# Performance work log

Measured on AMD Instinct MI355X. Metric: run time of the kernel, lower is better.

The kernel has to match this reference:

```python
import jax, jax.numpy as jnp
import numpy as np

B, F, V = 65536, 512, 28  # batch, feature_count, vocab_size (embedding hardcoded 28x28)


def setup_inputs() -> dict:
    key = jax.random.key(0)
    ks = jax.random.split(key, 12)
    s = lambda fan_in, fan_out: (2.0 / (fan_in + fan_out)) ** 0.5  # Glorot normal std
    return {
        "inputs": jax.random.normal(ks[0], (B, F), jnp.float32),
        "prev_prediction": jax.random.randint(ks[1], (B, V), 0, V, jnp.int32),
        "prev_state": jax.random.normal(ks[2], (B, V), jnp.float32),
        # GRUCell params (keras reset_after=True: two bias rows)
        "gru_kernel": jax.random.normal(ks[3], (F, 3 * V), jnp.float32) * s(F, 3 * V),
        "gru_rkernel": jax.random.normal(ks[4], (V, 3 * V), jnp.float32) * s(V, 3 * V),
        "gru_bias": jnp.zeros((2, 3 * V), jnp.float32),
        # cascaded output projections
        "Wo": jax.random.normal(ks[5], (V, 1), jnp.float32) * s(V, 1),
        "Uo": jax.random.normal(ks[6], (V, V), jnp.float32) * s(V, V),
        "Co": jax.random.normal(ks[7], (F, V), jnp.float32) * s(F, V),
        "Bo": jax.random.normal(ks[8], (1, V), jnp.float32) * s(1, V),
        "emb": jax.random.uniform(ks[9], (V, V), jnp.float32, -0.05, 0.05),
    }


def _gru_cell(x, h, kernel, rkernel, bias):
    # keras GRUCell, reset_after=True
    xm = x @ kernel + bias[0]          # [B, 3V]
    hm = h @ rkernel + bias[1]         # [B, 3V]
    xz, xr, xh = jnp.split(xm, 3, axis=-1)
    hz, hr, hh = jnp.split(hm, 3, axis=-1)
    z = jax.nn.sigmoid(xz + hz)
    r = jax.nn.sigmoid(xr + hr)
    hcand = jnp.tanh(xh + r * hh)
    return z * h + (1.0 - z) * hcand


def reference(inputs, prev_prediction, prev_state, gru_kernel, gru_rkernel, gru_bias, Wo, Uo, Co, Bo, emb):
    gru_out = _gru_cell(inputs, prev_state, gru_kernel, gru_rkernel, gru_bias)  # [B, V]
    emb_out = emb[prev_prediction]                      # [B, V, V] (gather)
    WoY = jnp.einsum("bve,e->bv", emb_out, Wo[:, 0])    # [B, V]
    UoH = prev_state @ Uo                               # [B, V]
    CoC = inputs @ Co                                   # [B, V]
    pred = jax.nn.softmax(WoY + UoH + CoC + Bo, axis=-1)
    return pred, gru_out
```

## Files before the change

kernel.cpp:

```cpp
#include <hip/hip_runtime.h>
#include <hip/hip_bf16.h>
#include <math.h>

#define BATCH   65536
#define FDIM    512
#define VDIM    28
#define TILE_R  64
#define NKS     32
#define W1N     (NKS * 4 * 64 * 8)
#define W2N     (2 * 4 * 64 * 8)


using short8 = __attribute__((ext_vector_type(8))) short;
using f32x16 = __attribute__((ext_vector_type(16))) float;

__device__ __forceinline__ float sigmoidf_(float x) { return 1.0f / (1.0f + __expf(-x)); }
__device__ __forceinline__ float tanhf_(float x) { return 1.0f - 2.0f / (1.0f + __expf(2.0f * x)); }

__device__ __forceinline__ unsigned short f2bf_rne(float f) {
    unsigned u = __float_as_uint(f);
    u += 0x7FFFu + ((u >> 16) & 1u);
    return (unsigned short)(u >> 16);
}

__device__ __forceinline__ void split2(float f0, float f1, unsigned& hp, unsigned& lp) {
    unsigned u0 = __float_as_uint(f0), u1 = __float_as_uint(f1);
    hp = (u0 >> 16) | (u1 & 0xFFFF0000u);
    float d0 = f0 - __uint_as_float(u0 & 0xFFFF0000u);
    float d1 = f1 - __uint_as_float(u1 & 0xFFFF0000u);
    unsigned v0 = __float_as_uint(d0), v1 = __float_as_uint(d1);
    lp = (v0 >> 16) | (v1 & 0xFFFF0000u);
}

__global__ void prep_kernel(const float* __restrict__ gk, const float* __restrict__ co,
                            const float* __restrict__ rk, const float* __restrict__ uo,
                            const float* __restrict__ emb, const float* __restrict__ wo,
                            unsigned short* __restrict__ w1h, unsigned short* __restrict__ w1l,
                            unsigned short* __restrict__ w2h, unsigned short* __restrict__ w2l,
                            float* __restrict__ tt) {
    int tid = blockIdx.x * 256 + threadIdx.x;
    int nth = gridDim.x * 256;
    for (int idx = tid; idx < W1N; idx += nth) {
        int j = idx & 7, lane = (idx >> 3) & 63, nf = (idx >> 9) & 3, ks = idx >> 11;
        int k = ks * 16 + ((lane >> 5) << 3) + j;
        int v = lane & 31;
        float val = 0.0f;
        if (v < VDIM) val = (nf < 3) ? gk[k * 84 + nf * 28 + v] : co[k * VDIM + v];
        unsigned short hi = f2bf_rne(val);
        float fh = __uint_as_float(((unsigned)hi) << 16);
        w1h[idx] = hi;
        w1l[idx] = f2bf_rne(val - fh);
    }
    for (int idx = tid; idx < W2N; idx += nth) {
        int j = idx & 7, lane = (idx >> 3) & 63, nf = (idx >> 9) & 3, ks = idx >> 11;
        int k = ks * 16 + ((lane >> 5) << 3) + j;
        int v = lane & 31;
        float val = 0.0f;
        if (v < VDIM && k < VDIM) val = (nf < 3) ? rk[k * 84 + nf * 28 + v] : uo[k * VDIM + v];
        unsigned short hi = f2bf_rne(val);
        float fh = __uint_as_float(((unsigned)hi) << 16);
        w2h[idx] = hi;
        w2l[idx] = f2bf_rne(val - fh);
    }
    if (tid < VDIM) {
        float s = 0.0f;
        for (int e = 0; e < VDIM; e++) s = fmaf(emb[tid * VDIM + e], wo[e], s);
        tt[tid] = s;
    }
}

#define MFMA(A, B, C) __builtin_amdgcn_mfma_f32_32x32x16_bf16(A, B, C, 0, 0, 0)
#define SPLIT8(A0, A1, AH, AL)                                        \
    {                                                                 \
        uint4 hu_, lu_;                                               \
        split2(A0.x, A0.y, hu_.x, lu_.x);                             \
        split2(A0.z, A0.w, hu_.y, lu_.y);                             \
        split2(A1.x, A1.y, hu_.z, lu_.z);                             \
        split2(A1.z, A1.w, hu_.w, lu_.w);                             \
        AH = __builtin_bit_cast(short8, hu_);                         \
        AL = __builtin_bit_cast(short8, lu_);                         \
    }
#define MFMA4(ACC, AH, AL, BH, BL)                                    \
    ACC = MFMA(AH, BH, ACC); ACC = MFMA(AL, BH, ACC);                 \
    ACC = MFMA(AH, BL, ACC); ACC = MFMA(AL, BL, ACC);

__global__ __launch_bounds__(128, 2) void gru_main_kernel(
    const float* __restrict__ x,
    const int*   __restrict__ pp,
    const float* __restrict__ ps,
    const float* __restrict__ bias,
    const float* __restrict__ bo,
    const unsigned short* __restrict__ w1h, const unsigned short* __restrict__ w1l,
    const unsigned short* __restrict__ w2h, const unsigned short* __restrict__ w2l,
    const float* __restrict__ tt,
    float* __restrict__ out)
{
    __shared__ float hbuf[TILE_R * VDIM];
    __shared__ int   ppbuf[TILE_R * VDIM];
    __shared__ float tts[32];

    const int t = threadIdx.x;
    const int wid = t >> 6, l = t & 63;
    const int cl = l & 31, gh = l >> 5;
    const long row0 = (long)blockIdx.x * TILE_R;
    const int m0 = 32 * wid;

    for (int i = t; i < TILE_R * VDIM; i += 128) {
        hbuf[i]  = ps[row0 * VDIM + i];
        ppbuf[i] = pp[row0 * VDIM + i];
    }
    if (t < 32) tts[t] = (t < VDIM) ? tt[t] : 0.0f;

    const int vc = (cl < VDIM) ? cl : (VDIM - 1);
    const float b0z = bias[vc],      b0r = bias[28 + vc],  b0h = bias[56 + vc];
    const float b1z = bias[84 + vc], b1r = bias[112 + vc], b1h = bias[140 + vc];
    const float bov = bo[vc];

    f32x16 accz = {}, accr = {}, acch = {}, accc = {}, hacch = {};

    {
        const float* hrow = ps + (row0 + m0 + cl) * (long)VDIM;
        const short8* bh8 = (const short8*)w2h + l;
        const short8* bl8 = (const short8*)w2l + l;
        short8 ah, al, bh, bl;
        {
            float4 a0 = *(const float4*)(hrow + gh * 8);
            float4 a1 = *(const float4*)(hrow + gh * 8 + 4);
            SPLIT8(a0, a1, ah, al);
            bh = bh8[0];   bl = bl8[0];   MFMA4(accz,  ah, al, bh, bl);
            bh = bh8[64];  bl = bl8[64];  MFMA4(accr,  ah, al, bh, bl);
            bh = bh8[128]; bl = bl8[128]; MFMA4(hacch, ah, al, bh, bl);
            bh = bh8[192]; bl = bl8[192]; MFMA4(accc,  ah, al, bh, bl);
        }
        {
            float4 a0 = *(const float4*)(hrow + 16 + gh * 8);
            float4 a1 = make_float4(0.f, 0.f, 0.f, 0.f);
            if (!gh) a1 = *(const float4*)(hrow + 20);
            SPLIT8(a0, a1, ah, al);
            bh = bh8[256]; bl = bl8[256]; MFMA4(accz,  ah, al, bh, bl);
            bh = bh8[320]; bl = bl8[320]; MFMA4(accr,  ah, al, bh, bl);
            bh = bh8[384]; bl = bl8[384]; MFMA4(hacch, ah, al, bh, bl);
            bh = bh8[448]; bl = bl8[448]; MFMA4(accc,  ah, al, bh, bl);
        }
    }

    {
        const float* xrow = x + (row0 + m0 + cl) * (long)FDIM + gh * 8;
        const short8* bh8 = (const short8*)w1h + l;
        const short8* bl8 = (const short8*)w1l + l;
        #pragma unroll 4
        for (int ks = 0; ks < NKS; ++ks) {
            float4 a0 = *(const float4*)(xrow + ks * 16);
            float4 a1 = *(const float4*)(xrow + ks * 16 + 4);
            short8 ah, al, bh, bl;
            SPLIT8(a0, a1, ah, al);
            const int kb = ks * 256;
            bh = bh8[kb];       bl = bl8[kb];       MFMA4(accz, ah, al, bh, bl);
            bh = bh8[kb + 64];  bl = bl8[kb + 64];  MFMA4(accr, ah, al, bh, bl);
            bh = bh8[kb + 128]; bl = bl8[kb + 128]; MFMA4(acch, ah, al, bh, bl);
            bh = bh8[kb + 192]; bl = bl8[kb + 192]; MFMA4(accc, ah, al, bh, bl);
        }
    }

    __syncthreads();

    #pragma unroll
    for (int r = 0; r < 16; ++r) {
        const int rowf = (r & 3) + ((r >> 2) << 3) + (gh << 2);
        const int grow = m0 + rowf;
        const long orow = row0 + grow;
        const float hp  = hbuf[grow * VDIM + vc];
        const int   ppv = ppbuf[grow * VDIM + vc];

        const float z  = sigmoidf_(accz[r] + b0z + b1z);
        const float rg = sigmoidf_(accr[r] + b0r + b1r);
        const float hc = tanhf_(acch[r] + b0h + rg * (hacch[r] + b1h));
        const float go = z * hp + (1.0f - z) * hc;
        const float logit = tts[ppv & 31] + accc[r] + bov;

        float mx = (cl < VDIM) ? logit : -1e30f;
        mx = fmaxf(mx, __shfl_xor(mx, 16));
        mx = fmaxf(mx, __shfl_xor(mx, 8));
        mx = fmaxf(mx, __shfl_xor(mx, 4));
        mx = fmaxf(mx, __shfl_xor(mx, 2));
        mx = fmaxf(mx, __shfl_xor(mx, 1));
        float p = (cl < VDIM) ? __expf(logit - mx) : 0.0f;
        float s = p;
        s += __shfl_xor(s, 16);
        s += __shfl_xor(s, 8);
        s += __shfl_xor(s, 4);
        s += __shfl_xor(s, 2);
        s += __shfl_xor(s, 1);

        if (cl < VDIM) {
            out[orow * VDIM + cl] = p / s;
            out[(long)BATCH * VDIM + orow * VDIM + cl] = go;
        }
    }
}

extern "C" void kernel_launch(void* const* d_in, const int* in_sizes, int n_in,
                              void* d_out, int out_size, void* d_ws, size_t ws_size,
                              hipStream_t stream) {
    const float* x    = (const float*)d_in[0];
    const int*   pp   = (const int*)  d_in[1];
    const float* ps   = (const float*)d_in[2];
    const float* gk   = (const float*)d_in[3];
    const float* rk   = (const float*)d_in[4];
    const float* bias = (const float*)d_in[5];
    const float* wo   = (const float*)d_in[6];
    const float* uo   = (const float*)d_in[7];
    const float* co   = (const float*)d_in[8];
    const float* bo   = (const float*)d_in[9];
    const float* emb  = (const float*)d_in[10];

    unsigned short* w1h = (unsigned short*)d_ws;
    unsigned short* w1l = w1h + W1N;
    unsigned short* w2h = w1l + W1N;
    unsigned short* w2l = w2h + W2N;
    float*          tt  = (float*)(w2l + W2N);

    prep_kernel<<<64, 256, 0, stream>>>(gk, co, rk, uo, emb, wo, w1h, w1l, w2h, w2l, tt);
    gru_main_kernel<<<BATCH / TILE_R, 128, 0, stream>>>(
        x, pp, ps, bias, bo, w1h, w1l, w2h, w2l, tt, (float*)d_out);
}
```

Measured before the change: 257.3 us.

## Split K across warps and double-buffer weight tiles via global_load_lds

Doubles the block to 256 threads, with two warps per 32-row group each taking half of the 512-wide K range. Weight fragments are streamed into double-buffered LDS with async global-to-LDS loads, and x loads are prefetched one step ahead. Partial accumulators are then reduced through LDS before a single warp does the epilogue. The aim is more latency hiding and parallelism on a load-bound GEMM, at the cost of a barrier every K step plus five reduction barriers, and the epilogue now reads prev_state and prev_prediction straight from global memory.

```diff
diff --git a/kernel.cpp b/kernel.cpp
--- a/kernel.cpp
+++ b/kernel.cpp
@@ -6,10 +6,8 @@
 #define FDIM    512
 #define VDIM    28
 #define TILE_R  64
-#define NKS     32
-#define W1N     (NKS * 4 * 64 * 8)
+#define W1N     (32 * 4 * 64 * 8)
 #define W2N     (2 * 4 * 64 * 8)
-
 
 using short8 = __attribute__((ext_vector_type(8))) short;
 using f32x16 = __attribute__((ext_vector_type(16))) float;
@@ -84,7 +82,11 @@
     ACC = MFMA(AH, BH, ACC); ACC = MFMA(AL, BH, ACC);                 \
     ACC = MFMA(AH, BL, ACC); ACC = MFMA(AL, BL, ACC);
 
-__global__ __launch_bounds__(128, 2) void gru_main_kernel(
+#define GLD_LDS16(G, L) __builtin_amdgcn_global_load_lds(                         \
+    (const __attribute__((address_space(1))) void*)(G),                           \
+    (__attribute__((address_space(3))) void*)(L), 16, 0, 0)
+
+__global__ __launch_bounds__(256, 3) void gru_main_kernel(
     const float* __restrict__ x,
     const int*   __restrict__ pp,
     const float* __restrict__ ps,
@@ -95,21 +97,21 @@
     const float* __restrict__ tt,
     float* __restrict__ out)
 {
-    __shared__ float hbuf[TILE_R * VDIM];
-    __shared__ int   ppbuf[TILE_R * VDIM];
-    __shared__ float tts[32];
+    __shared__ short8 bb[2][2][2][256];
 
     const int t = threadIdx.x;
     const int wid = t >> 6, l = t & 63;
+    const int wid_m = wid & 1, wid_k = wid >> 1;
     const int cl = l & 31, gh = l >> 5;
     const long row0 = (long)blockIdx.x * TILE_R;
-    const int m0 = 32 * wid;
-
-    for (int i = t; i < TILE_R * VDIM; i += 128) {
-        hbuf[i]  = ps[row0 * VDIM + i];
-        ppbuf[i] = pp[row0 * VDIM + i];
-    }
-    if (t < 32) tts[t] = (t < VDIM) ? tt[t] : 0.0f;
+    const int m0x = 32 * wid_m;
+
+    #pragma unroll
+    for (int rr = 0; rr < 4; ++rr) {
+        const int s = rr >> 1, p = rr & 1;
+        const unsigned short* srcb = p ? w1l : w1h;
+        GLD_LDS16(srcb + (s * 16) * 2048 + t * 8, &bb[s][0][p][t]);
+    }
 
     const int vc = (cl < VDIM) ? cl : (VDIM - 1);
     const float b0z = bias[vc],      b0r = bias[28 + vc],  b0h = bias[56 + vc];
@@ -118,83 +120,114 @@
 
     f32x16 accz = {}, accr = {}, acch = {}, accc = {}, hacch = {};
 
+    const float* xrow = x + (row0 + m0x + cl) * (long)FDIM + gh * 8;
+    const int ks0 = wid_k * 16;
+    float4 a0n = *(const float4*)(xrow + ks0 * 16);
+    float4 a1n = *(const float4*)(xrow + ks0 * 16 + 4);
+
     {
-        const float* hrow = ps + (row0 + m0 + cl) * (long)VDIM;
+        const float* hrow = ps + (row0 + m0x + cl) * (long)VDIM;
         const short8* bh8 = (const short8*)w2h + l;
         const short8* bl8 = (const short8*)w2l + l;
+        float4 a0, a1;
+        if (wid_k == 0) {
+            a0 = *(const float4*)(hrow + gh * 8);
+            a1 = *(const float4*)(hrow + gh * 8 + 4);
+        } else {
+            a0 = *(const float4*)(hrow + 16 + gh * 8);
+            a1 = make_float4(0.f, 0.f, 0.f, 0.f);
+            if (!gh) a1 = *(const float4*)(hrow + 20);
+        }
         short8 ah, al, bh, bl;
-        {
-            float4 a0 = *(const float4*)(hrow + gh * 8);
-            float4 a1 = *(const float4*)(hrow + gh * 8 + 4);
-            SPLIT8(a0, a1, ah, al);
-            bh = bh8[0];   bl = bl8[0];   MFMA4(accz,  ah, al, bh, bl);
-            bh = bh8[64];  bl = bl8[64];  MFMA4(accr,  ah, al, bh, bl);
-            bh = bh8[128]; bl = bl8[128]; MFMA4(hacch, ah, al, bh, bl);
-            bh = bh8[192]; bl = bl8[192]; MFMA4(accc,  ah, al, bh, bl);
+        SPLIT8(a0, a1, ah, al);
+        const int ko = wid_k * 256;
+        bh = bh8[ko];       bl = bl8[ko];       MFMA4(accz,  ah, al, bh, bl);
+        bh = bh8[ko + 64];  bl = bl8[ko + 64];  MFMA4(accr,  ah, al, bh, bl);
+        bh = bh8[ko + 128]; bl = bl8[ko + 128]; MFMA4(hacch, ah, al, bh, bl);
+        bh = bh8[ko + 192]; bl = bl8[ko + 192]; MFMA4(accc,  ah, al, bh, bl);
+    }
+
+    __syncthreads();
+
+    #pragma unroll
+    for (int i = 0; i < 16; ++i) {
+        float4 a0c = a0n, a1c = a1n;
+        if (i + 1 < 16) {
+            a0n = *(const float4*)(xrow + (ks0 + i + 1) * 16);
+            a1n = *(const float4*)(xrow + (ks0 + i + 1) * 16 + 4);
+            #pragma unroll
+            for (int rr = 0; rr < 4; ++rr) {
+                const int s = rr >> 1, p = rr & 1;
+                const unsigned short* srcb = p ? w1l : w1h;
+                GLD_LDS16(srcb + (s * 16 + i + 1) * 2048 + t * 8,
+                          &bb[s][(i + 1) & 1][p][t]);
+            }
         }
-        {
-            float4 a0 = *(const float4*)(hrow + 16 + gh * 8);
-            float4 a1 = make_float4(0.f, 0.f, 0.f, 0.f);
-            if (!gh) a1 = *(const float4*)(hrow + 20);
-            SPLIT8(a0, a1, ah, al);
-            bh = bh8[256]; bl = bl8[256]; MFMA4(accz,  ah, al, bh, bl);
-            bh = bh8[320]; bl = bl8[320]; MFMA4(accr,  ah, al, bh, bl);
-            bh = bh8[384]; bl = bl8[384]; MFMA4(hacch, ah, al, bh, bl);
-            bh = bh8[448]; bl = bl8[448]; MFMA4(accc,  ah, al, bh, bl);
-        }
-    }
-
-    {
-        const float* xrow = x + (row0 + m0 + cl) * (long)FDIM + gh * 8;
-        const short8* bh8 = (const short8*)w1h + l;
-        const short8* bl8 = (const short8*)w1l + l;
-        #pragma unroll 4
-        for (int ks = 0; ks < NKS; ++ks) {
-            float4 a0 = *(const float4*)(xrow + ks * 16);
-            float4 a1 = *(const float4*)(xrow + ks * 16 + 4);
-            short8 ah, al, bh, bl;
-            SPLIT8(a0, a1, ah, al);
-            const int kb = ks * 256;
-            bh = bh8[kb];       bl = bl8[kb];       MFMA4(accz, ah, al, bh, bl);
-            bh = bh8[kb + 64];  bl = bl8[kb + 64];  MFMA4(accr, ah, al, bh, bl);
-            bh = bh8[kb + 128]; bl = bl8[kb + 128]; MFMA4(acch, ah, al, bh, bl);
-            bh = bh8[kb + 192]; bl = bl8[kb + 192]; MFMA4(accc, ah, al, bh, bl);
-        }
-    }
-
+        short8 ah, al;
+        SPLIT8(a0c, a1c, ah, al);
+        const short8* Bh = &bb[wid_k][i & 1][0][0];
+        const short8* Bl = &bb[wid_k][i & 1][1][0];
+        short8 bh, bl;
+        bh = Bh[l];        bl = Bl[l];        MFMA4(accz, ah, al, bh, bl);
+        bh = Bh[64 + l];   bl = Bl[64 + l];   MFMA4(accr, ah, al, bh, bl);
+        bh = Bh[128 + l];  bl = Bl[128 + l];  MFMA4(acch, ah, al, bh, bl);
+        bh = Bh[192 + l];  bl = Bl[192 + l];  MFMA4(accc, ah, al, bh, bl);
+        __syncthreads();
+    }
+
+    float* rbuf = (float*)&bb[0][0][0][0];
+#define REDUCE(ACC)                                                              \
+    if (wid_k == 1) {                                                            \
+        _Pragma("unroll")                                                        \
+        for (int r = 0; r < 16; ++r) rbuf[(wid_m * 16 + r) * 64 + l] = ACC[r];   \
+    }                                                                            \
+    __syncthreads();                                                             \
+    if (wid_k == 0) {                                                            \
+        _Pragma("unroll")                                                        \
+        for (int r = 0; r < 16; ++r) ACC[r] += rbuf[(wid_m * 16 + r) * 64 + l];  \
+    }                                                                            \
     __syncthreads();
 
-    #pragma unroll
-    for (int r = 0; r < 16; ++r) {
-        const int rowf = (r & 3) + ((r >> 2) << 3) + (gh << 2);
-        const int grow = m0 + rowf;
-        const long orow = row0 + grow;
-        const float hp  = hbuf[grow * VDIM + vc];
-        const int   ppv = ppbuf[grow * VDIM + vc];
-
-        const float z  = sigmoidf_(accz[r] + b0z + b1z);
-        const float rg = sigmoidf_(accr[r] + b0r + b1r);
-        const float hc = tanhf_(acch[r] + b0h + rg * (hacch[r] + b1h));
-        const float go = z * hp + (1.0f - z) * hc;
-        const float logit = tts[ppv & 31] + accc[r] + bov;
-
-        float mx = (cl < VDIM) ? logit : -1e30f;
-        mx = fmaxf(mx, __shfl_xor(mx, 16));
-        mx = fmaxf(mx, __shfl_xor(mx, 8));
-        mx = fmaxf(mx, __shfl_xor(mx, 4));
-        mx = fmaxf(mx, __shfl_xor(mx, 2));
-        mx = fmaxf(mx, __shfl_xor(mx, 1));
-        float p = (cl < VDIM) ? __expf(logit - mx) : 0.0f;
-        float s = p;
-        s += __shfl_xor(s, 16);
-        s += __shfl_xor(s, 8);
-        s += __shfl_xor(s, 4);
-        s += __shfl_xor(s, 2);
-        s += __shfl_xor(s, 1);
-
-        if (cl < VDIM) {
-            out[orow * VDIM + cl] = p / s;
-            out[(long)BATCH * VDIM + orow * VDIM + cl] = go;
+    REDUCE(accz)
+    REDUCE(accr)
+    REDUCE(acch)
+    REDUCE(hacch)
+    REDUCE(accc)
+#undef REDUCE
+
+    if (wid_k == 0) {
+        #pragma unroll
+        for (int r = 0; r < 16; ++r) {
+            const int rowf = (r & 3) + ((r >> 2) << 3) + (gh << 2);
+            const long orow = row0 + m0x + rowf;
+            const float hp  = ps[orow * VDIM + vc];
+            const int   ppv = pp[orow * VDIM + vc];
+            const float ttv = tt[ppv];
+
+            const float z  = sigmoidf_(accz[r] + b0z + b1z);
+            const float rg = sigmoidf_(accr[r] + b0r + b1r);
+            const float hc = tanhf_(acch[r] + b0h + rg * (hacch[r] + b1h));
+            const float go = z * hp + (1.0f - z) * hc;
+            const float logit = ttv + accc[r] + bov;
+
+            float mx = (cl < VDIM) ? logit : -1e30f;
+            mx = fmaxf(mx, __shfl_xor(mx, 16));
+            mx = fmaxf(mx, __shfl_xor(mx, 8));
+            mx = fmaxf(mx, __shfl_xor(mx, 4));
+            mx = fmaxf(mx, __shfl_xor(mx, 2));
+            mx = fmaxf(mx, __shfl_xor(mx, 1));
+            float p = (cl < VDIM) ? __expf(logit - mx) : 0.0f;
+            float s = p;
+            s += __shfl_xor(s, 16);
+            s += __shfl_xor(s, 8);
+            s += __shfl_xor(s, 4);
+            s += __shfl_xor(s, 2);
+            s += __shfl_xor(s, 1);
+
+            if (cl < VDIM) {
+                out[orow * VDIM + cl] = p / s;
+                out[(long)BATCH * VDIM + orow * VDIM + cl] = go;
+            }
         }
     }
 }
@@ -220,7 +253,7 @@
     unsigned short* w2l = w2h + W2N;
     float*          tt  = (float*)(w2l + W2N);
 
-    prep_kernel<<<64, 256, 0, stream>>>(gk, co, rk, uo, emb, wo, w1h, w1l, w2h, w2l, tt);
-    gru_main_kernel<<<BATCH / TILE_R, 128, 0, stream>>>(
+    prep_kernel<<<256, 256, 0, stream>>>(gk, co, rk, uo, emb, wo, w1h, w1l, w2h, w2l, tt);
+    gru_main_kernel<<<BATCH / TILE_R, 256, 0, stream>>>(
         x, pp, ps, bias, bo, w1h, w1l, w2h, w2l, tt, (float*)d_out);
 }
```

New measurement: 254.7 us. No clear change (-1.0%).
